# Performance work log

Measured on AMD Instinct MI355X. Metric: run time of the kernel, lower is better.

## Reference

```python
import jax, jax.numpy as jnp
import numpy as np

B = 16        # batch
N = 1024      # satellite nodes
D = 256       # hidden size
H = 8         # attention heads
NUM_LAYERS = 3          # config.n_layer_aa
L = NUM_LAYERS + 1      # distinct GAT layers
EPS = 1e-5


def setup_inputs() -> dict:
    key = jax.random.key(0)
    ks = jax.random.split(key, 6)
    graph_vectors = jax.random.normal(ks[0], (B, N + 1, D), dtype=jnp.float32)
    graph = jax.random.uniform(ks[1], (B, N, N), dtype=jnp.float32)
    scale = 0.02
    Wq = jax.random.normal(ks[2], (L, D, D), dtype=jnp.float32) * scale
    Wk = jax.random.normal(ks[3], (L, D, D), dtype=jnp.float32) * scale
    Wv = jax.random.normal(ks[4], (L, D, D), dtype=jnp.float32) * scale
    Wo = jax.random.normal(ks[5], (L, D, D), dtype=jnp.float32) * scale
    ln_g = jnp.ones((L, D), dtype=jnp.float32)
    ln_b = jnp.zeros((L, D), dtype=jnp.float32)
    return {"graph_vectors": graph_vectors, "graph": graph,
            "Wq": Wq, "Wk": Wk, "Wv": Wv, "Wo": Wo,
            "ln_g": ln_g, "ln_b": ln_b}


def _layer_norm(x, g, b):
    mu = jnp.mean(x, axis=-1, keepdims=True)
    var = jnp.var(x, axis=-1, keepdims=True)
    return (x - mu) * jax.lax.rsqrt(var + EPS) * g + b


def _gat(x_q, x_kv, wq, wk, wv, wo, g, b):
    # multi-head attention: x_q [B,Lq,D] attends over x_kv [B,Lk,D]
    Bq, Lq, _ = x_q.shape
    Lk = x_kv.shape[1]
    dh = D // H
    q = (x_q @ wq).reshape(Bq, Lq, H, dh)
    k = (x_kv @ wk).reshape(Bq, Lk, H, dh)
    v = (x_kv @ wv).reshape(Bq, Lk, H, dh)
    scores = jnp.einsum('bqhd,bkhd->bhqk', q, k) / jnp.sqrt(jnp.float32(dh))
    attn = jax.nn.softmax(scores, axis=-1)
    o = jnp.einsum('bhqk,bkhd->bqhd', attn, v).reshape(Bq, Lq, D)
    out = o @ wo
    return _layer_norm(out + x_q, g, b)


def reference(graph_vectors, graph, Wq, Wk, Wv, Wo, ln_g, ln_b):
    relay = graph_vectors[:, :1, :]        # [B,1,D]
    sat = graph_vectors[:, 1:, :]          # [B,N,D]
    # layer 0: relay attends over satellites
    relay = _gat(relay, sat, Wq[0], Wk[0], Wv[0], Wo[0], ln_g[0], ln_b[0])
    # satellite = (satellite^T @ graph)^T -> [B,N,D]
    sat = jnp.einsum('bnd,bnm->bmd', sat, graph)
    gv = jnp.concatenate([relay, sat], axis=1)   # [B,N+1,D]
    # middle layers: full self-attention over all N+1 nodes
    for i in range(1, NUM_LAYERS):
        gv = _gat(gv, gv, Wq[i], Wk[i], Wv[i], Wo[i], ln_g[i], ln_b[i])
    relay_u = gv[:, :1, :]
    sat_u = gv[:, 1:, :]
    z = _gat(relay_u, sat_u, Wq[-1], Wk[-1], Wv[-1], Wo[-1], ln_g[-1], ln_b[-1])[:, 0, :]
    return z, sat_u
```

## Files before the change

### kernel.cpp

```cpp
#include <hip/hip_runtime.h>
#include <hip/hip_bf16.h>
#include <math.h>

#define BD   256
#define NH   8
#define DH   32
#define NB   16
#define NN   1024
#define LQ   1025
#define EPSV 1e-5f
#define KP   1088

typedef unsigned short ushort_t;
typedef __attribute__((ext_vector_type(8))) short short8;
typedef __attribute__((ext_vector_type(4))) float f32x4;

static __device__ __forceinline__ ushort_t f2b(float x) {
  union { __hip_bfloat16 h; ushort_t u; } cv;
  cv.h = __float2bfloat16(x);
  return cv.u;
}
static __device__ __forceinline__ float b2f(ushort_t u) {
  union { float f; unsigned v; } c; c.v = ((unsigned)u) << 16; return c.f;
}
static __device__ __forceinline__ float fexp2(float x) {
#if defined(__has_builtin)
#if __has_builtin(__builtin_amdgcn_exp2f)
  return __builtin_amdgcn_exp2f(x);
#else
  return exp2f(x);
#endif
#else
  return exp2f(x);
#endif
}

__global__ void k_copy_cast(const float* __restrict__ in, float* __restrict__ X,
                            ushort_t* __restrict__ Xh, long n) {
  long stride = (long)gridDim.x * 256;
  for (long i = (long)blockIdx.x * 256 + threadIdx.x; i < n; i += stride) {
    float v = in[i];
    X[i] = v;
    Xh[i] = f2b(v);
  }
}

__global__ void k_sat_out(const float* __restrict__ X, float* __restrict__ out) {
  long n = (long)NB * NN * BD;
  long stride = (long)gridDim.x * 256;
  for (long i = (long)blockIdx.x * 256 + threadIdx.x; i < n; i += stride) {
    long b = i / ((long)NN * BD);
    long r = i - b * ((long)NN * BD);
    out[i] = X[b * (long)LQ * BD + BD + r];
  }
}

__global__ __launch_bounds__(256) void k_wtrans(const float* __restrict__ Wq,
                                                const float* __restrict__ Wk,
                                                const float* __restrict__ Wv,
                                                const float* __restrict__ Wo,
                                                ushort_t* __restrict__ Wt) {
  const float C1 = 0.17677669529663687f * 1.4426950408889634f;
  int mat = blockIdx.y;
  int type = mat >> 2, layer = mat & 3;
  const float* src = (type == 0) ? Wq : (type == 1) ? Wk : (type == 2) ? Wv : Wo;
  src += (long)layer * BD * BD;
  float scv = (type == 0) ? C1 : 1.f;
  ushort_t* dst = Wt + (long)mat * BD * BD;
  __shared__ float t[32][33];
  int k0 = (blockIdx.x & 7) * 32, n0 = (blockIdx.x >> 3) * 32;
  int tid = threadIdx.x;
  for (int i = tid; i < 1024; i += 256) {
    int kk = i >> 5, nn = i & 31;
    t[kk][nn] = src[(long)(k0 + kk) * BD + n0 + nn];
  }
  __syncthreads();
  for (int i = tid; i < 1024; i += 256) {
    int nn = i >> 5, kk = i & 31;
    dst[(long)(n0 + nn) * BD + k0 + kk] = f2b(t[kk][nn] * scv);
  }
}

__global__ __launch_bounds__(256) void k_gtrans(const float* __restrict__ G,
                                                ushort_t* __restrict__ Ght) {
  __shared__ ushort_t t[64][65];
  int b = blockIdx.y;
  int m0 = (blockIdx.x & 15) * 64, n0 = (blockIdx.x >> 4) * 64;
  const float* Gb = G + (long)b * NN * NN;
  ushort_t* dst = Ght + (long)b * NN * NN;
  int tid = threadIdx.x;
  #pragma unroll
  for (int rr = 0; rr < 16; rr++) {
    int n = rr * 4 + (tid >> 6);
    int m = tid & 63;
    t[m][n] = f2b(Gb[(long)(n0 + n) * NN + m0 + m]);
  }
  __syncthreads();
  #pragma unroll
  for (int rr = 0; rr < 8; rr++) {
    int m = rr * 8 + (tid >> 5);
    int n2 = (tid & 31) * 2;
    unsigned w = (unsigned)t[m][n2] | ((unsigned)t[m][n2 + 1] << 16);
    *(unsigned*)&dst[(long)(m0 + m) * NN + n0 + n2] = w;
  }
}

__global__ __launch_bounds__(256) void k_satT(const ushort_t* __restrict__ Xh,
                                              ushort_t* __restrict__ satT) {
  __shared__ ushort_t t[64][65];
  int b = blockIdx.y;
  int n0 = (blockIdx.x & 15) * 64, d0 = (blockIdx.x >> 4) * 64;
  const ushort_t* src = Xh + ((long)b * LQ + 1) * BD;
  ushort_t* dst = satT + (long)b * BD * NN;
  int tid = threadIdx.x;
  #pragma unroll
  for (int rr = 0; rr < 16; rr++) {
    int n = rr * 4 + (tid >> 6);
    int d = tid & 63;
    t[n][d] = src[(long)(n0 + n) * BD + d0 + d];
  }
  __syncthreads();
  #pragma unroll
  for (int rr = 0; rr < 8; rr++) {
    int d = rr * 8 + (tid >> 5);
    int n2 = (tid & 31) * 2;
    unsigned w = (unsigned)t[n2][d] | ((unsigned)t[n2 + 1][d] << 16);
    *(unsigned*)&dst[(long)(d0 + d) * NN + n0 + n2] = w;
  }
}

__global__ __launch_bounds__(256) void k_vtrans(const ushort_t* __restrict__ Vh,
                                                ushort_t* __restrict__ VhT) {
  __shared__ ushort_t t[64][65];
  int b = blockIdx.z;
  int n0 = blockIdx.x * 64, d0 = blockIdx.y * 64;
  const ushort_t* src = Vh + (long)b * LQ * BD;
  ushort_t* dst = VhT + (long)b * BD * KP;
  int tid = threadIdx.x;
  #pragma unroll
  for (int rr = 0; rr < 16; rr++) {
    int n = rr * 4 + (tid >> 6);
    int d = tid & 63;
    int key = n0 + n;
    t[n][d] = (key < LQ) ? src[(long)key * BD + d0 + d] : (ushort_t)0;
  }
  __syncthreads();
  #pragma unroll
  for (int rr = 0; rr < 8; rr++) {
    int d = rr * 8 + (tid >> 5);
    int n2 = (tid & 31) * 2;
    unsigned w = (unsigned)t[n2][d] | ((unsigned)t[n2 + 1][d] << 16);
    *(unsigned*)&dst[(long)(d0 + d) * KP + n0 + n2] = w;
  }
}

static __device__ __forceinline__ void gemm_core(const ushort_t* __restrict__ A,
                                                 const ushort_t* __restrict__ W,
                                                 ushort_t* Ws,
                                                 float* __restrict__ Cf,
                                                 ushort_t* __restrict__ Ch,
                                                 int M, int m0, int n0) {
  int tid = threadIdx.x;
  int wave = tid >> 6, lane = tid & 63;
  int l15 = lane & 15, quad = lane >> 4;
  for (int i = tid; i < 64 * 32; i += 256) {
    int r = i >> 5, c8 = (i & 31) * 8;
    *(uint4*)&Ws[r * 264 + c8] = *(const uint4*)&W[(long)(n0 + r) * 256 + c8];
  }
  __syncthreads();
  int mrow = m0 + wave * 16 + l15;
  if (mrow > M - 1) mrow = M - 1;
  f32x4 acc[4];
  #pragma unroll
  for (int f = 0; f < 4; f++) { acc[f][0] = 0.f; acc[f][1] = 0.f; acc[f][2] = 0.f; acc[f][3] = 0.f; }
  #pragma unroll
  for (int k0 = 0; k0 < 256; k0 += 32) {
    short8 a = *(const short8*)&A[(long)mrow * 256 + k0 + quad * 8];
    #pragma unroll
    for (int f = 0; f < 4; f++) {
      short8 bb = *(const short8*)&Ws[(f * 16 + l15) * 264 + k0 + quad * 8];
      acc[f] = __builtin_amdgcn_mfma_f32_16x16x32_bf16(a, bb, acc[f], 0, 0, 0);
    }
  }
  #pragma unroll
  for (int f = 0; f < 4; f++)
    #pragma unroll
    for (int r = 0; r < 4; r++) {
      int m = m0 + wave * 16 + quad * 4 + r;
      if (m < M) {
        long idx = (long)m * 256 + n0 + f * 16 + l15;
        if (Cf) Cf[idx] = acc[f][r];
        else    Ch[idx] = f2b(acc[f][r]);
      }
    }
}

__global__ __launch_bounds__(256) void gemm_qkv(const ushort_t* __restrict__ Xh,
                                                const ushort_t* __restrict__ Wt, int layer,
                                                ushort_t* __restrict__ Qo,
                                                ushort_t* __restrict__ Ko,
                                                ushort_t* __restrict__ Vo, int M) {
  __shared__ __align__(16) ushort_t Ws[64 * 264];
  int which = blockIdx.y >> 2, n0 = (blockIdx.y & 3) * 64;
  const ushort_t* W = Wt + (long)(which * 4 + layer) * 65536;
  ushort_t* C = (which == 0) ? Qo : (which == 1) ? Ko : Vo;
  gemm_core(Xh, W, Ws, nullptr, C, M, blockIdx.x * 64, n0);
}

__global__ __launch_bounds__(256) void gemm_kv(const ushort_t* __restrict__ Xh,
                                               const ushort_t* __restrict__ Wt, int layer,
                                               ushort_t* __restrict__ Ko,
                                               ushort_t* __restrict__ Vo) {
  __shared__ __align__(16) ushort_t Ws[64 * 264];
  int which = blockIdx.y >> 2, n0 = (blockIdx.y & 3) * 64;
  int b = blockIdx.z;
  const ushort_t* W = Wt + (long)((which + 1) * 4 + layer) * 65536;
  const ushort_t* A = Xh + (long)b * (LQ * BD) + BD;
  ushort_t* C = ((which == 0) ? Ko : Vo) + (long)b * (NN * BD);
  gemm_core(A, W, Ws, nullptr, C, NN, blockIdx.x * 64, n0);
}

__global__ __launch_bounds__(256) void gemm_oproj(const ushort_t* __restrict__ Oh,
                                                  const ushort_t* __restrict__ Wt, int layer,
                                                  float* __restrict__ Cf, int M) {
  __shared__ __align__(16) ushort_t Ws[64 * 264];
  gemm_core(Oh, Wt + (long)(12 + layer) * 65536, Ws, Cf, nullptr, M,
            blockIdx.x * 64, blockIdx.y * 64);
}

__global__ __launch_bounds__(256) void gemm_gtx2(const ushort_t* __restrict__ Ght,
                                                 const ushort_t* __restrict__ satT,
                                                 float* __restrict__ X,
                                                 ushort_t* __restrict__ Xh) {
  __shared__ __align__(16) ushort_t As[128 * 72];
  __shared__ __align__(16) ushort_t Bs[128 * 72];
  int b = blockIdx.z;
  const ushort_t* A  = Ght + (long)b * NN * NN;
  const ushort_t* Bp = satT + (long)b * BD * NN;
  int tid = threadIdx.x;
  int wave = tid >> 6, lane = tid & 63;
  int l15 = lane & 15, quad = lane >> 4;
  int wr = wave >> 1, wc = wave & 1;
  int m0 = blockIdx.x * 128, d0 = blockIdx.y * 128;

  int sr = tid >> 2, sc = (tid & 3) * 8;
  const ushort_t* aSrc0 = A  + (long)(m0 + sr) * NN + sc;
  const ushort_t* aSrc1 = aSrc0 + (long)64 * NN;
  const ushort_t* bSrc0 = Bp + (long)(d0 + sr) * NN + sc;
  const ushort_t* bSrc1 = bSrc0 + (long)64 * NN;
  ushort_t* aDst0 = &As[sr * 72 + sc];
  ushort_t* aDst1 = aDst0 + 64 * 72;
  ushort_t* bDst0 = &Bs[sr * 72 + sc];
  ushort_t* bDst1 = bDst0 + 64 * 72;

  {
    uint4 a0 = *(const uint4*)aSrc0;
    uint4 a1 = *(const uint4*)aSrc1;
    uint4 b0 = *(const uint4*)bSrc0;
    uint4 b1 = *(const uint4*)bSrc1;
    *(uint4*)aDst0 = a0; *(uint4*)aDst1 = a1;
    *(uint4*)bDst0 = b0; *(uint4*)bDst1 = b1;
  }
  __syncthreads();

  f32x4 acc[4][4];
  #pragma unroll
  for (int i = 0; i < 4; i++)
    #pragma unroll
    for (int j = 0; j < 4; j++) { acc[i][j][0] = 0.f; acc[i][j][1] = 0.f; acc[i][j][2] = 0.f; acc[i][j][3] = 0.f; }

  for (int ks = 0; ks < 32; ks++) {
    bool more = (ks < 31);
    uint4 na0, na1, nb0, nb1;
    if (more) {
      aSrc0 += 32; aSrc1 += 32; bSrc0 += 32; bSrc1 += 32;
      na0 = *(const uint4*)aSrc0;
      na1 = *(const uint4*)aSrc1;
      nb0 = *(const uint4*)bSrc0;
      nb1 = *(const uint4*)bSrc1;
    }
    short8 af[4], bf[4];
    #pragma unroll
    for (int f = 0; f < 4; f++)
      af[f] = *(const short8*)&As[(wr * 64 + f * 16 + l15) * 72 + quad * 8];
    #pragma unroll
    for (int f = 0; f < 4; f++)
      bf[f] = *(const short8*)&Bs[(wc * 64 + f * 16 + l15) * 72 + quad * 8];
    #pragma unroll
    for (int i = 0; i < 4; i++)
      #pragma unroll
      for (int j = 0; j < 4; j++)
        acc[i][j] = __builtin_amdgcn_mfma_f32_16x16x32_bf16(af[i], bf[j], acc[i][j], 0, 0, 0);
    if (more) {
      __syncthreads();
      *(uint4*)aDst0 = na0;
      *(uint4*)aDst1 = na1;
      *(uint4*)bDst0 = nb0;
      *(uint4*)bDst1 = nb1;
      __syncthreads();
    }
  }

  long xb = ((long)b * LQ + 1) * 256;
  #pragma unroll
  for (int i = 0; i < 4; i++)
    #pragma unroll
    for (int j = 0; j < 4; j++)
      #pragma unroll
      for (int r = 0; r < 4; r++) {
        int m = m0 + wr * 64 + i * 16 + quad * 4 + r;
        int d = d0 + wc * 64 + j * 16 + l15;
        long idx = xb + (long)m * 256 + d;
        X[idx] = acc[i][j][r];
        Xh[idx] = f2b(acc[i][j][r]);
      }
}

__global__ __launch_bounds__(256) void attn_fa(const ushort_t* __restrict__ Qh,
                                               const ushort_t* __restrict__ Kh,
                                               const ushort_t* __restrict__ VhT,
                                               ushort_t* __restrict__ Oh) {
  __shared__ __align__(16) ushort_t Ps[4][32][72];
  __shared__ __align__(16) ushort_t Kb[64 * 72];
  __shared__ __align__(16) ushort_t Vb[32 * 72];
  __shared__ float Lbuf[4][32];
  int tid = threadIdx.x;
  int wave = tid >> 6, lane = tid & 63;
  int l15 = lane & 15, quad = lane >> 4;
  int b = blockIdx.x >> 3, h = blockIdx.x & 7;
  long hb = ((long)b * LQ) * BD + h * DH;
  long vB = (long)b * BD * KP;
  int hd0 = h * DH;
  int q0 = blockIdx.y * 128 + wave * 32;
  int lq = lane & 48;

  short8 qB[2];
  #pragma unroll
  for (int t = 0; t < 2; t++) {
    int qc = q0 + t * 16 + l15; if (qc > LQ - 1) qc = LQ - 1;
    qB[t] = *(const short8*)&Qh[hb + (long)qc * BD + quad * 8];
  }

  const ushort_t *s0, *s1;
  ushort_t *d0, *d1;
  long stp;
  if (wave < 2) {
    int kt0 = wave * 2, kt1 = kt0 + 1;
    s0 = Kh + hb + (long)(kt0 * 16 + l15) * BD + quad * 8;
    s1 = Kh + hb + (long)(kt1 * 16 + l15) * BD + quad * 8;
    d0 = &Kb[(kt0 * 16 + l15) * 72 + quad * 8];
    d1 = &Kb[(kt1 * 16 + l15) * 72 + quad * 8];
    stp = (long)64 * BD;
  } else {
    int sa = (wave - 2) * 2, sb = sa + 1;
    s0 = VhT + vB + (long)(hd0 + (sa >> 1) * 16 + l15) * KP + (sa & 1) * 32 + quad * 8;
    s1 = VhT + vB + (long)(hd0 + (sb >> 1) * 16 + l15) * KP + (sb & 1) * 32 + quad * 8;
    d0 = &Vb[((sa >> 1) * 16 + l15) * 72 + (sa & 1) * 32 + quad * 8];
    d1 = &Vb[((sb >> 1) * 16 + l15) * 72 + (sb & 1) * 32 + quad * 8];
    stp = 64;
  }
  {
    uint4 r0 = *(const uint4*)s0;
    uint4 r1 = *(const uint4*)s1;
    *(uint4*)d0 = r0;
    *(uint4*)d1 = r1;
  }
  __syncthreads();

  f32x4 o[2][2];
  #pragma unroll
  for (int t = 0; t < 2; t++)
    #pragma unroll
    for (int dt = 0; dt < 2; dt++) { o[t][dt][0] = 0.f; o[t][dt][1] = 0.f; o[t][dt][2] = 0.f; o[t][dt][3] = 0.f; }
  float m[2] = {-1e30f, -1e30f};
  float ls[2] = {0.f, 0.f};
  f32x4 zf; zf[0] = 0.f; zf[1] = 0.f; zf[2] = 0.f; zf[3] = 0.f;

  for (int c = 0; c < 17; c++) {
    bool more = (c < 16);
    uint4 n0, n1;
    if (more) {
      if (c == 15 && wave < 2) {
        const ushort_t* cl = Kh + hb + (long)(LQ - 1) * BD + quad * 8;
        n0 = *(const uint4*)cl;
        n1 = n0;
      } else {
        s0 += stp; s1 += stp;
        n0 = *(const uint4*)s0;
        n1 = *(const uint4*)s1;
      }
    }
    short8 ka[4];
    #pragma unroll
    for (int kt = 0; kt < 4; kt++)
      ka[kt] = *(const short8*)&Kb[(kt * 16 + l15) * 72 + quad * 8];

    bool tail = (c == 16);
    #pragma unroll
    for (int t = 0; t < 2; t++) {
      f32x4 s[4];
      #pragma unroll
      for (int kt = 0; kt < 4; kt++)
        s[kt] = __builtin_amdgcn_mfma_f32_16x16x32_bf16(ka[kt], qB[t], zf, 0, 0, 0);
      if (tail) {
        #pragma unroll
        for (int kt = 0; kt < 4; kt++)
          #pragma unroll
          for (int r = 0; r < 4; r++)
            if (kt + r) s[kt][r] = -1e30f;
        if (quad) s[0][0] = -1e30f;
      }
      float cm = fmaxf(fmaxf(s[0][0], s[0][1]), fmaxf(s[0][2], s[0][3]));
      cm = fmaxf(cm, fmaxf(fmaxf(s[1][0], s[1][1]), fmaxf(s[1][2], s[1][3])));
      cm = fmaxf(cm, fmaxf(fmaxf(s[2][0], s[2][1]), fmaxf(s[2][2], s[2][3])));
      cm = fmaxf(cm, fmaxf(fmaxf(s[3][0], s[3][1]), fmaxf(s[3][2], s[3][3])));
      cm = fmaxf(cm, __shfl_xor(cm, 16));
      cm = fmaxf(cm, __shfl_xor(cm, 32));
      if (__any(cm > m[t] + 8.f)) {
        float mn = fmaxf(m[t], cm);
        float f = fexp2(m[t] - mn);
        ls[t] *= f;
        m[t] = mn;
        #pragma unroll
        for (int r = 0; r < 4; r++) {
          float fr = __shfl(f, lq | (quad * 4 + r));
          o[t][0][r] *= fr;
          o[t][1][r] *= fr;
        }
      }
      float mt = m[t];
      #pragma unroll
      for (int kt = 0; kt < 4; kt++) {
        float p0 = fexp2(s[kt][0] - mt);
        float p1 = fexp2(s[kt][1] - mt);
        float p2 = fexp2(s[kt][2] - mt);
        float p3 = fexp2(s[kt][3] - mt);
        ls[t] += (p0 + p1) + (p2 + p3);
        unsigned lo = (unsigned)f2b(p0) | ((unsigned)f2b(p1) << 16);
        unsigned hi = (unsigned)f2b(p2) | ((unsigned)f2b(p3) << 16);
        uint2 w; w.x = lo; w.y = hi;
        *(uint2*)&Ps[wave][t * 16 + l15][kt * 16 + quad * 4] = w;
      }
    }
    short8 vb[2][2];
    #pragma unroll
    for (int dt = 0; dt < 2; dt++)
      #pragma unroll
      for (int ks = 0; ks < 2; ks++)
        vb[ks][dt] = *(const short8*)&Vb[(dt * 16 + l15) * 72 + ks * 32 + quad * 8];
    #pragma unroll
    for (int ks = 0; ks < 2; ks++) {
      short8 pa0 = *(const short8*)&Ps[wave][l15][ks * 32 + quad * 8];
      short8 pa1 = *(const short8*)&Ps[wave][16 + l15][ks * 32 + quad * 8];
      #pragma unroll
      for (int dt = 0; dt < 2; dt++) {
        o[0][dt] = __builtin_amdgcn_mfma_f32_16x16x32_bf16(pa0, vb[ks][dt], o[0][dt], 0, 0, 0);
        o[1][dt] = __builtin_amdgcn_mfma_f32_16x16x32_bf16(pa1, vb[ks][dt], o[1][dt], 0, 0, 0);
      }
    }
    if (more) {
      __syncthreads();
      *(uint4*)d0 = n0;
      *(uint4*)d1 = n1;
      __syncthreads();
    }
  }
  #pragma unroll
  for (int t = 0; t < 2; t++) {
    ls[t] += __shfl_xor(ls[t], 16);
    ls[t] += __shfl_xor(ls[t], 32);
  }
  if (quad == 0) {
    Lbuf[wave][l15] = ls[0];
    Lbuf[wave][16 + l15] = ls[1];
  }
  __syncthreads();
  #pragma unroll
  for (int mt = 0; mt < 2; mt++) {
    f32x4 lv = *(const f32x4*)&Lbuf[wave][mt * 16 + quad * 4];
    #pragma unroll
    for (int r = 0; r < 4; r++) {
      int row = q0 + mt * 16 + quad * 4 + r;
      if (row < LQ) {
        float den = lv[r];
        float inv = (den > 0.f) ? 1.f / den : 0.f;
        #pragma unroll
        for (int dt = 0; dt < 2; dt++)
          Oh[hb + (long)row * BD + dt * 16 + l15] = f2b(o[mt][dt][r] * inv);
      }
    }
  }
}

__global__ __launch_bounds__(256) void attn_relay(const float* __restrict__ q,
                                                  const ushort_t* __restrict__ K,
                                                  const ushort_t* __restrict__ V,
                                                  float* __restrict__ o) {
  int b = blockIdx.x, h = blockIdx.y;
  int tid = threadIdx.x;
  const float scale = 0.17677669529663687f;
  __shared__ float s[NN];
  __shared__ float qs[DH];
  __shared__ float rbuf[256];
  __shared__ float part[8][33];
  if (tid < DH) qs[tid] = q[(long)b * BD + h * DH + tid];
  __syncthreads();
  long base = ((long)b * NN) * BD + h * DH;
  for (int k = tid; k < NN; k += 256) {
    float dot = 0.f;
    const ushort_t* kr = &K[base + (long)k * BD];
    #pragma unroll
    for (int d2 = 0; d2 < 16; d2++) {
      unsigned w = *(const unsigned*)&kr[d2 * 2];
      dot += qs[d2 * 2] * b2f((ushort_t)(w & 0xffff)) + qs[d2 * 2 + 1] * b2f((ushort_t)(w >> 16));
    }
    s[k] = dot * scale;
  }
  __syncthreads();
  float m = -1e30f;
  for (int k = tid; k < NN; k += 256) m = fmaxf(m, s[k]);
  rbuf[tid] = m;
  __syncthreads();
  for (int st = 128; st > 0; st >>= 1) {
    if (tid < st) rbuf[tid] = fmaxf(rbuf[tid], rbuf[tid + st]);
    __syncthreads();
  }
  float mx = rbuf[0];
  __syncthreads();
  float sm = 0.f;
  for (int k = tid; k < NN; k += 256) {
    float p = __expf(s[k] - mx);
    s[k] = p;
    sm += p;
  }
  rbuf[tid] = sm;
  __syncthreads();
  for (int st = 128; st > 0; st >>= 1) {
    if (tid < st) rbuf[tid] += rbuf[tid + st];
    __syncthreads();
  }
  float inv = 1.f / rbuf[0];
  int d = tid & 31, slice = tid >> 5;
  float acc = 0.f;
  for (int k = slice; k < NN; k += 8) acc += s[k] * b2f(V[base + (long)k * BD + d]);
  part[slice][d] = acc;
  __syncthreads();
  if (tid < DH) {
    float ss = 0.f;
    #pragma unroll
    for (int t = 0; t < 8; t++) ss += part[t][tid];
    o[(long)b * BD + h * DH + tid] = ss * inv;
  }
}

__global__ __launch_bounds__(256) void rowvec_matmul(const float* __restrict__ X, long xstride,
                                                     const float* __restrict__ W,
                                                     float* __restrict__ out) {
  int b = blockIdx.x, tid = threadIdx.x;
  __shared__ float xs[BD];
  xs[tid] = X[(long)b * xstride + tid];
  __syncthreads();
  float acc = 0.f;
  for (int k = 0; k < BD; k++) acc += xs[k] * W[(long)k * BD + tid];
  out[(long)b * BD + tid] = acc;
}

__global__ __launch_bounds__(256) void rowvec_oproj_ln(const float* __restrict__ o,
                                                       const float* __restrict__ Wo,
                                                       const float* __restrict__ Xres, long xstride,
                                                       const float* __restrict__ g,
                                                       const float* __restrict__ beta,
                                                       float* __restrict__ dst, long dstride,
                                                       ushort_t* __restrict__ dsth, long dhstride) {
  int b = blockIdx.x, tid = threadIdx.x;
  __shared__ float xs[BD];
  __shared__ float rs[256], rq[256];
  xs[tid] = o[(long)b * BD + tid];
  __syncthreads();
  float acc = 0.f;
  for (int k = 0; k < BD; k++) acc += xs[k] * Wo[(long)k * BD + tid];
  float v = acc + Xres[(long)b * xstride + tid];
  rs[tid] = v;
  rq[tid] = v * v;
  __syncthreads();
  for (int st = 128; st > 0; st >>= 1) {
    if (tid < st) { rs[tid] += rs[tid + st]; rq[tid] += rq[tid + st]; }
    __syncthreads();
  }
  float mu = rs[0] * (1.f / BD);
  float var = rq[0] * (1.f / BD) - mu * mu;
  float y = (v - mu) * rsqrtf(var + EPSV) * g[tid] + beta[tid];
  dst[(long)b * dstride + tid] = y;
  if (dsth) dsth[(long)b * dhstride + tid] = f2b(y);
}

__global__ __launch_bounds__(256) void ln_residual(const float* __restrict__ OP,
                                                   float* __restrict__ X,
                                                   ushort_t* __restrict__ Xh,
                                                   const float* __restrict__ g,
                                                   const float* __restrict__ beta) {
  long r = blockIdx.x;
  int tid = threadIdx.x;
  __shared__ float rs[256], rq[256];
  float v = OP[r * BD + tid] + X[r * BD + tid];
  rs[tid] = v;
  rq[tid] = v * v;
  __syncthreads();
  for (int st = 128; st > 0; st >>= 1) {
    if (tid < st) { rs[tid] += rs[tid + st]; rq[tid] += rq[tid + st]; }
    __syncthreads();
  }
  float mu = rs[0] * (1.f / BD);
  float var = rq[0] * (1.f / BD) - mu * mu;
  float y = (v - mu) * rsqrtf(var + EPSV) * g[tid] + beta[tid];
  X[r * BD + tid] = y;
  Xh[r * BD + tid] = f2b(y);
}

extern "C" void kernel_launch(void* const* d_in, const int* in_sizes, int n_in,
                              void* d_out, int out_size, void* d_ws, size_t ws_size,
                              hipStream_t stream) {
  const float* gv    = (const float*)d_in[0];
  const float* graph = (const float*)d_in[1];
  const float* Wq    = (const float*)d_in[2];
  const float* Wk    = (const float*)d_in[3];
  const float* Wv    = (const float*)d_in[4];
  const float* Wo    = (const float*)d_in[5];
  const float* lg    = (const float*)d_in[6];
  const float* lb    = (const float*)d_in[7];
  float* out = (float*)d_out;

  const long S  = (long)NB * LQ * BD;
  const long S4 = S * 4, S2 = S * 2;
  char* base = (char*)d_ws;
  float*    X    = (float*)base;
  ushort_t* Xh   = (ushort_t*)(base + S4);
  float*    B1   = (float*)(base + S4 + S2);
  ushort_t* Qh   = (ushort_t*)(base + 2 * S4 + S2);
  ushort_t* Kh   = (ushort_t*)(base + 2 * S4 + 2 * S2);
  ushort_t* Vh   = (ushort_t*)(base + 2 * S4 + 3 * S2);
  ushort_t* Oh   = (ushort_t*)(base + 2 * S4 + 4 * S2);
  ushort_t* Wt   = (ushort_t*)(base + 2 * S4 + 5 * S2);
  float*    qrel = (float*)(base + 2 * S4 + 5 * S2 + 16L * 65536 * 2);
  float*    orel = qrel + (long)NB * BD;
  ushort_t* Ght  = (ushort_t*)B1;
  ushort_t* satT = Vh;
  ushort_t* VhT  = (ushort_t*)B1;

  const long WSZ = (long)BD * BD;
  const long XST = (long)LQ * BD;
  dim3 blk(256);

  k_copy_cast<<<dim3(2048), blk, 0, stream>>>(gv, X, Xh, S);
  k_wtrans<<<dim3(64, 16), blk, 0, stream>>>(Wq, Wk, Wv, Wo, Wt);

  rowvec_matmul<<<dim3(NB), blk, 0, stream>>>(X, XST, Wq + 0 * WSZ, qrel);
  gemm_kv<<<dim3(16, 8, NB), blk, 0, stream>>>(Xh, Wt, 0, Kh, Vh);
  attn_relay<<<dim3(NB, NH), blk, 0, stream>>>(qrel, Kh, Vh, orel);
  rowvec_oproj_ln<<<dim3(NB), blk, 0, stream>>>(orel, Wo + 0 * WSZ, X, XST,
                                                lg + 0 * BD, lb + 0 * BD, X, XST, Xh, XST);

  k_gtrans<<<dim3(256, NB), blk, 0, stream>>>(graph, Ght);
  k_satT<<<dim3(64, NB), blk, 0, stream>>>(Xh, satT);
  gemm_gtx2<<<dim3(8, 2, NB), blk, 0, stream>>>(Ght, satT, X, Xh);

  for (int l = 1; l <= 2; l++) {
    gemm_qkv<<<dim3(257, 12), blk, 0, stream>>>(Xh, Wt, l, Qh, Kh, Vh, NB * LQ);
    k_vtrans<<<dim3(17, 4, NB), blk, 0, stream>>>(Vh, VhT);
    attn_fa<<<dim3(NB * NH, 9), blk, 0, stream>>>(Qh, Kh, VhT, Oh);
    gemm_oproj<<<dim3(257, 4), blk, 0, stream>>>(Oh, Wt, l, B1, NB * LQ);
    ln_residual<<<dim3(NB * LQ), blk, 0, stream>>>(B1, X, Xh, lg + l * BD, lb + l * BD);
  }

  k_sat_out<<<dim3(2048), blk, 0, stream>>>(X, out + (long)NB * BD);

  rowvec_matmul<<<dim3(NB), blk, 0, stream>>>(X, XST, Wq + 3 * WSZ, qrel);
  gemm_kv<<<dim3(16, 8, NB), blk, 0, stream>>>(Xh, Wt, 3, Kh, Vh);
  attn_relay<<<dim3(NB, NH), blk, 0, stream>>>(qrel, Kh, Vh, orel);
  rowvec_oproj_ln<<<dim3(NB), blk, 0, stream>>>(orel, Wo + 3 * WSZ, X, XST,
                                                lg + 3 * BD, lb + 3 * BD, out, BD, nullptr, 0);
}
```

Measured before the change: 553.6 us.

## Retile QKV GEMM to 128x128 blocks and compute softmax row sums via MFMA

After: 541.3 us. -2.2%, faster.

```diff
diff --git a/kernel.cpp b/kernel.cpp
--- a/kernel.cpp
+++ b/kernel.cpp
@@ -200,11 +200,90 @@
                                                 ushort_t* __restrict__ Qo,
                                                 ushort_t* __restrict__ Ko,
                                                 ushort_t* __restrict__ Vo, int M) {
-  __shared__ __align__(16) ushort_t Ws[64 * 264];
-  int which = blockIdx.y >> 2, n0 = (blockIdx.y & 3) * 64;
+  __shared__ __align__(16) ushort_t As[128 * 72];
+  __shared__ __align__(16) ushort_t Bs[128 * 72];
+  int tid = threadIdx.x;
+  int wave = tid >> 6, lane = tid & 63;
+  int l15 = lane & 15, quad = lane >> 4;
+  int wr = wave >> 1, wc = wave & 1;
+  int which = blockIdx.y >> 1;
+  int n0 = (blockIdx.y & 1) * 128;
   const ushort_t* W = Wt + (long)(which * 4 + layer) * 65536;
   ushort_t* C = (which == 0) ? Qo : (which == 1) ? Ko : Vo;
-  gemm_core(Xh, W, Ws, nullptr, C, M, blockIdx.x * 64, n0);
+  int m0 = blockIdx.x * 128;
+
+  int sr = tid >> 2, sc = (tid & 3) * 8;
+  int ar0 = m0 + sr;      if (ar0 > M - 1) ar0 = M - 1;
+  int ar1 = m0 + sr + 64; if (ar1 > M - 1) ar1 = M - 1;
+  const ushort_t* aSrc0 = Xh + (long)ar0 * 256 + sc;
+  const ushort_t* aSrc1 = Xh + (long)ar1 * 256 + sc;
+  const ushort_t* bSrc0 = W + (long)(n0 + sr) * 256 + sc;
+  const ushort_t* bSrc1 = bSrc0 + 64 * 256;
+  ushort_t* aDst0 = &As[sr * 72 + sc];
+  ushort_t* aDst1 = aDst0 + 64 * 72;
+  ushort_t* bDst0 = &Bs[sr * 72 + sc];
+  ushort_t* bDst1 = bDst0 + 64 * 72;
+
+  {
+    uint4 a0 = *(const uint4*)aSrc0;
+    uint4 a1 = *(const uint4*)aSrc1;
+    uint4 b0 = *(const uint4*)bSrc0;
+    uint4 b1 = *(const uint4*)bSrc1;
+    *(uint4*)aDst0 = a0; *(uint4*)aDst1 = a1;
+    *(uint4*)bDst0 = b0; *(uint4*)bDst1 = b1;
+  }
+  __syncthreads();
+
+  f32x4 acc[4][4];
+  #pragma unroll
+  for (int i = 0; i < 4; i++)
+    #pragma unroll
+    for (int j = 0; j < 4; j++) { acc[i][j][0] = 0.f; acc[i][j][1] = 0.f; acc[i][j][2] = 0.f; acc[i][j][3] = 0.f; }
+
+  for (int ks = 0; ks < 8; ks++) {
+    bool more = (ks < 7);
+    uint4 na0, na1, nb0, nb1;
+    if (more) {
+      aSrc0 += 32; aSrc1 += 32; bSrc0 += 32; bSrc1 += 32;
+      na0 = *(const uint4*)aSrc0;
+      na1 = *(const uint4*)aSrc1;
+      nb0 = *(const uint4*)bSrc0;
+      nb1 = *(const uint4*)bSrc1;
+    }
+    short8 af[4], bf[4];
+    #pragma unroll
+    for (int f = 0; f < 4; f++)
+      af[f] = *(const short8*)&As[(wr * 64 + f * 16 + l15) * 72 + quad * 8];
+    #pragma unroll
+    for (int f = 0; f < 4; f++)
+      bf[f] = *(const short8*)&Bs[(wc * 64 + f * 16 + l15) * 72 + quad * 8];
+    #pragma unroll
+    for (int i = 0; i < 4; i++)
+      #pragma unroll
+      for (int j = 0; j < 4; j++)
+        acc[i][j] = __builtin_amdgcn_mfma_f32_16x16x32_bf16(af[i], bf[j], acc[i][j], 0, 0, 0);
+    if (more) {
+      __syncthreads();
+      *(uint4*)aDst0 = na0;
+      *(uint4*)aDst1 = na1;
+      *(uint4*)bDst0 = nb0;
+      *(uint4*)bDst1 = nb1;
+      __syncthreads();
+    }
+  }
+
+  #pragma unroll
+  for (int i = 0; i < 4; i++)
+    #pragma unroll
+    for (int j = 0; j < 4; j++)
+      #pragma unroll
+      for (int r = 0; r < 4; r++) {
+        int m = m0 + wr * 64 + i * 16 + quad * 4 + r;
+        if (m < M) {
+          int n = n0 + wc * 64 + j * 16 + l15;
+          C[(long)m * 256 + n] = f2b(acc[i][j][r]);
+        }
+      }
 }
 
 __global__ __launch_bounds__(256) void gemm_kv(const ushort_t* __restrict__ Xh,
@@ -323,7 +402,6 @@
   __shared__ __align__(16) ushort_t Ps[4][32][72];
   __shared__ __align__(16) ushort_t Kb[64 * 72];
   __shared__ __align__(16) ushort_t Vb[32 * 72];
-  __shared__ float Lbuf[4][32];
   int tid = threadIdx.x;
   int wave = tid >> 6, lane = tid & 63;
   int l15 = lane & 15, quad = lane >> 4;
@@ -340,6 +418,10 @@
     int qc = q0 + t * 16 + l15; if (qc > LQ - 1) qc = LQ - 1;
     qB[t] = *(const short8*)&Qh[hb + (long)qc * BD + quad * 8];
   }
+
+  short8 onesB;
+  #pragma unroll
+  for (int i = 0; i < 8; i++) onesB[i] = (short)0x3F80;
 
   const ushort_t *s0, *s1;
   ushort_t *d0, *d1;
@@ -372,8 +454,10 @@
   for (int t = 0; t < 2; t++)
     #pragma unroll
     for (int dt = 0; dt < 2; dt++) { o[t][dt][0] = 0.f; o[t][dt][1] = 0.f; o[t][dt][2] = 0.f; o[t][dt][3] = 0.f; }
+  f32x4 lsa[2];
+  lsa[0][0] = 0.f; lsa[0][1] = 0.f; lsa[0][2] = 0.f; lsa[0][3] = 0.f;
+  lsa[1][0] = 0.f; lsa[1][1] = 0.f; lsa[1][2] = 0.f; lsa[1][3] = 0.f;
   float m[2] = {-1e30f, -1e30f};
-  float ls[2] = {0.f, 0.f};
   f32x4 zf; zf[0] = 0.f; zf[1] = 0.f; zf[2] = 0.f; zf[3] = 0.f;
 
   for (int c = 0; c < 17; c++) {
@@ -419,13 +503,13 @@
       if (__any(cm > m[t] + 8.f)) {
         float mn = fmaxf(m[t], cm);
         float f = fexp2(m[t] - mn);
-        ls[t] *= f;
         m[t] = mn;
         #pragma unroll
         for (int r = 0; r < 4; r++) {
           float fr = __shfl(f, lq | (quad * 4 + r));
           o[t][0][r] *= fr;
           o[t][1][r] *= fr;
+          lsa[t][r] *= fr;
         }
       }
       float mt = m[t];
@@ -435,7 +519,6 @@
         float p1 = fexp2(s[kt][1] - mt);
         float p2 = fexp2(s[kt][2] - mt);
         float p3 = fexp2(s[kt][3] - mt);
-        ls[t] += (p0 + p1) + (p2 + p3);
         unsigned lo = (unsigned)f2b(p0) | ((unsigned)f2b(p1) << 16);
         unsigned hi = (unsigned)f2b(p2) | ((unsigned)f2b(p3) << 16);
         uint2 w; w.x = lo; w.y = hi;
@@ -452,6 +535,8 @@
     for (int ks = 0; ks < 2; ks++) {
       short8 pa0 = *(const short8*)&Ps[wave][l15][ks * 32 + quad * 8];
       short8 pa1 = *(const short8*)&Ps[wave][16 + l15][ks * 32 + quad * 8];
+      lsa[0] = __builtin_amdgcn_mfma_f32_16x16x32_bf16(pa0, onesB, lsa[0], 0, 0, 0);
+      lsa[1] = __builtin_amdgcn_mfma_f32_16x16x32_bf16(pa1, onesB, lsa[1], 0, 0, 0);
       #pragma unroll
       for (int dt = 0; dt < 2; dt++) {
         o[0][dt] = __builtin_amdgcn_mfma_f32_16x16x32_bf16(pa0, vb[ks][dt], o[0][dt], 0, 0, 0);
@@ -466,23 +551,12 @@
     }
   }
   #pragma unroll
-  for (int t = 0; t < 2; t++) {
-    ls[t] += __shfl_xor(ls[t], 16);
-    ls[t] += __shfl_xor(ls[t], 32);
-  }
-  if (quad == 0) {
-    Lbuf[wave][l15] = ls[0];
-    Lbuf[wave][16 + l15] = ls[1];
-  }
-  __syncthreads();
-  #pragma unroll
   for (int mt = 0; mt < 2; mt++) {
-    f32x4 lv = *(const f32x4*)&Lbuf[wave][mt * 16 + quad * 4];
     #pragma unroll
     for (int r = 0; r < 4; r++) {
       int row = q0 + mt * 16 + quad * 4 + r;
       if (row < LQ) {
-        float den = lv[r];
+        float den = lsa[mt][r];
         float inv = (den > 0.f) ? 1.f / den : 0.f;
         #pragma unroll
         for (int dt = 0; dt < 2; dt++)
@@ -665,7 +739,7 @@
   gemm_gtx2<<<dim3(8, 2, NB), blk, 0, stream>>>(Ght, satT, X, Xh);
 
   for (int l = 1; l <= 2; l++) {
-    gemm_qkv<<<dim3(257, 12), blk, 0, stream>>>(Xh, Wt, l, Qh, Kh, Vh, NB * LQ);
+    gemm_qkv<<<dim3(129, 6), blk, 0, stream>>>(Xh, Wt, l, Qh, Kh, Vh, NB * LQ);
     k_vtrans<<<dim3(17, 4, NB), blk, 0, stream>>>(Vh, VhT);
     attn_fa<<<dim3(NB * NH, 9), blk, 0, stream>>>(Qh, Kh, VhT, Oh);
     gemm_oproj<<<dim3(257, 4), blk, 0, stream>>>(Oh, Wt, l, B1, NB * LQ);
```
